# Optimization experiments

Hardware: AMD Instinct MI355X
Metric: run time of the kernel (lower is better)

Reference implementation:

```python
import jax, jax.numpy as jnp
import numpy as np

NUM_HEADS = 32
NUM_KV_HEADS = 8
HEAD_DIM = 128
HIDDEN = 4096
ROPE_THETA = 10000.0
RMS_EPS = 1e-6


def setup_inputs() -> dict:
    key = jax.random.key(0)
    k1, k2, k3 = jax.random.split(key, 3)
    T = 2048
    qkv_out = (NUM_HEADS + 2 * NUM_KV_HEADS) * HEAD_DIM  # 6144
    return {
        "positions": jnp.arange(T, dtype=jnp.int64),
        "hidden_states": jax.random.normal(k1, (T, HIDDEN), dtype=jnp.float32),
        "wqkv": jax.random.normal(k2, (qkv_out, HIDDEN), dtype=jnp.float32) * 0.02,
        "wo": jax.random.normal(k3, (HIDDEN, NUM_HEADS * HEAD_DIM), dtype=jnp.float32) * 0.02,
        "q_norm_w": jnp.ones((HEAD_DIM,), dtype=jnp.float32),
        "k_norm_w": jnp.ones((HEAD_DIM,), dtype=jnp.float32),
    }


def _rms_norm(x, w):
    # per-head RMSNorm over last dim, computed in fp32 (matches Dots1RMSNorm)
    xf = x.astype(jnp.float32)
    var = jnp.mean(xf * xf, axis=-1, keepdims=True)
    return (w * (xf * jax.lax.rsqrt(var + RMS_EPS))).astype(x.dtype)


def _rope(x, positions):
    # NeoX-style rotary: rotate halves. x: [T, H, D]
    half = HEAD_DIM // 2
    inv_freq = 1.0 / (ROPE_THETA ** (jnp.arange(0, half, dtype=jnp.float32) / half))
    ang = positions.astype(jnp.float32)[:, None] * inv_freq  # [T, half]
    cos = jnp.cos(ang)[:, None, :]  # [T,1,half]
    sin = jnp.sin(ang)[:, None, :]
    x1, x2 = x[..., :half], x[..., half:]
    return jnp.concatenate([x1 * cos - x2 * sin, x2 * cos + x1 * sin], axis=-1)


def reference(positions, hidden_states, wqkv, wo, q_norm_w, k_norm_w):
    T = hidden_states.shape[0]
    q_size = NUM_HEADS * HEAD_DIM
    kv_size = NUM_KV_HEADS * HEAD_DIM
    qkv = hidden_states @ wqkv.T  # [T, q_size + 2*kv_size]
    q = qkv[:, :q_size].reshape(T, NUM_HEADS, HEAD_DIM)
    k = qkv[:, q_size:q_size + kv_size].reshape(T, NUM_KV_HEADS, HEAD_DIM)
    v = qkv[:, q_size + kv_size:].reshape(T, NUM_KV_HEADS, HEAD_DIM)

    q = _rms_norm(q, q_norm_w)
    k = _rms_norm(k, k_norm_w)
    q = _rope(q, positions)
    k = _rope(k, positions)

    # GQA: expand kv heads to query heads (group of 4)
    group = NUM_HEADS // NUM_KV_HEADS
    k = jnp.repeat(k, group, axis=1)  # [T, H, D]
    v = jnp.repeat(v, group, axis=1)

    scale = HEAD_DIM ** -0.5
    scores = jnp.einsum('thd,shd->hts', q, k) * scale  # [H, T, T]
    causal = positions[:, None] >= positions[None, :]
    scores = jnp.where(causal[None, :, :], scores, jnp.finfo(scores.dtype).min)
    probs = jax.nn.softmax(scores, axis=-1)
    attn = jnp.einsum('hts,shd->thd', probs, v)  # [T, H, D]
    out = attn.reshape(T, NUM_HEADS * HEAD_DIM) @ wo.T  # [T, HIDDEN]
    return out
```

## Files before the change

kernel.cpp:

```cpp
#include <hip/hip_runtime.h>


#define T_SEQ 2048
#define HID   4096
#define NH    32
#define NKVH  8
#define HD    128
#define QKVN  6144
#define QSZ   4096
#define QKN   5120

typedef unsigned short u16;
typedef __attribute__((ext_vector_type(8))) short short8;
typedef __attribute__((ext_vector_type(4))) float floatx4;

__device__ __forceinline__ float bf2f(u16 u) {
  union { unsigned int i; float f; } c; c.i = ((unsigned int)u) << 16; return c.f;
}
__device__ __forceinline__ u16 f2bf(float f) {
  union { float f; unsigned int i; } c; c.f = f;
  unsigned int u = c.i;
  return (u16)((u + 0x7FFFu + ((u >> 16) & 1u)) >> 16);
}
__device__ __forceinline__ floatx4 mfma16(short8 a, short8 b, floatx4 c) {
  return __builtin_amdgcn_mfma_f32_16x16x32_bf16(a, b, c, 0, 0, 0);
}

#define GLD16(g, l) __builtin_amdgcn_global_load_lds( \
    (__attribute__((address_space(1))) unsigned int*)(g), \
    (__attribute__((address_space(3))) unsigned int*)(l), 16, 0, 0)

__global__ __launch_bounds__(256) void cvt3_kernel(
    const float* __restrict__ s0, const float* __restrict__ s1,
    const float* __restrict__ s2, u16* __restrict__ d0, u16* __restrict__ d1,
    u16* __restrict__ d2, int n0, int n1, int n2) {
  int total = n0 + n1 + n2;
  int stride = gridDim.x * 256;
  for (int i = blockIdx.x * 256 + threadIdx.x; i < total; i += stride) {
    const float* s; u16* d; int j = i;
    if (j < n0)           { s = s0; d = d0; }
    else if (j < n0 + n1) { j -= n0; s = s1; d = d1; }
    else                  { j -= n0 + n1; s = s2; d = d2; }
    float4 v = ((const float4*)s)[j];
    ushort4 o;
    o.x = f2bf(v.x); o.y = f2bf(v.y); o.z = f2bf(v.z); o.w = f2bf(v.w);
    ((ushort4*)d)[j] = o;
  }
}

template <int MODE>
__global__ __launch_bounds__(256, 2) void gemm_bt(const u16* __restrict__ A,
    const u16* __restrict__ B, void* __restrict__ Cv, u16* __restrict__ VT,
    int mtiles, int K, int ldC) {
  __shared__ __attribute__((aligned(16))) u16 As[128 * 64];
  __shared__ __attribute__((aligned(16))) u16 Bs[128 * 64];
  const int tid = threadIdx.x;
  const int wave = tid >> 6, lane = tid & 63;
  const int lq = lane >> 4, lc = lane & 15;
  const int wm = wave >> 1, wn = wave & 1;
  const int by = blockIdx.x % mtiles, bx = blockIdx.x / mtiles;
  const int m0 = by * 128, n0 = bx * 128;

  floatx4 acc[4][4];
#pragma unroll
  for (int i = 0; i < 4; ++i)
#pragma unroll
    for (int j = 0; j < 4; ++j) acc[i][j] = {0.f, 0.f, 0.f, 0.f};

  int arow[4], brow[4];
#pragma unroll
  for (int i = 0; i < 4; ++i) {
    arow[i] = wm * 64 + i * 16 + lc;
    brow[i] = wn * 64 + i * 16 + lc;
  }

  const u16* asrc[4]; const u16* bsrc[4];
#pragma unroll
  for (int r = 0; r < 4; ++r) {
    int L = r * 256 + tid;
    int mm = L >> 3;
    int cc = (L & 7) ^ (mm & 7);
    asrc[r] = A + (size_t)(m0 + mm) * K + cc * 8;
    bsrc[r] = B + (size_t)(n0 + mm) * K + cc * 8;
  }

  for (int k0 = 0; k0 < K; k0 += 64) {
#pragma unroll
    for (int r = 0; r < 4; ++r) {
      GLD16(asrc[r] + k0, As + (r * 256 + wave * 64) * 8);
      GLD16(bsrc[r] + k0, Bs + (r * 256 + wave * 64) * 8);
    }
    __syncthreads();
#pragma unroll
    for (int kb = 0; kb < 2; ++kb) {
      short8 af[4], bfr[4];
#pragma unroll
      for (int mi = 0; mi < 4; ++mi)
        af[mi] = *(const short8*)&As[arow[mi] * 64 + (((kb * 4 + lq) ^ (arow[mi] & 7)) * 8)];
#pragma unroll
      for (int ni = 0; ni < 4; ++ni)
        bfr[ni] = *(const short8*)&Bs[brow[ni] * 64 + (((kb * 4 + lq) ^ (brow[ni] & 7)) * 8)];
#pragma unroll
      for (int mi = 0; mi < 4; ++mi)
#pragma unroll
        for (int ni = 0; ni < 4; ++ni)
          acc[mi][ni] = mfma16(af[mi], bfr[ni], acc[mi][ni]);
    }
    __syncthreads();
  }

  if (MODE == 1 && n0 >= 5120) {
#pragma unroll
    for (int mi = 0; mi < 4; ++mi) {
      int row = m0 + wm * 64 + mi * 16 + lq * 4;
#pragma unroll
      for (int ni = 0; ni < 4; ++ni) {
        int rel = n0 + wn * 64 + ni * 16 + lc - 5120;
        ushort4 u;
        u.x = f2bf(acc[mi][ni][0]); u.y = f2bf(acc[mi][ni][1]);
        u.z = f2bf(acc[mi][ni][2]); u.w = f2bf(acc[mi][ni][3]);
        *(ushort4*)&VT[(size_t)rel * T_SEQ + row] = u;
      }
    }
  } else {
#pragma unroll
    for (int mi = 0; mi < 4; ++mi) {
      int row = m0 + wm * 64 + mi * 16 + lq * 4;
#pragma unroll
      for (int ni = 0; ni < 4; ++ni) {
        int col = n0 + wn * 64 + ni * 16 + lc;
#pragma unroll
        for (int r = 0; r < 4; ++r) {
          if (MODE == 1)
            ((u16*)Cv)[(size_t)(row + r) * ldC + col] = f2bf(acc[mi][ni][r]);
          else
            ((float*)Cv)[(size_t)(row + r) * ldC + col] = acc[mi][ni][r];
        }
      }
    }
  }
}

__global__ __launch_bounds__(256) void norm_rope_kernel(const u16* __restrict__ qk,
    const float* __restrict__ qw, const float* __restrict__ kw,
    u16* __restrict__ Qo, u16* __restrict__ Ko) {
  const int t = blockIdx.x;
  const int hs = blockIdx.y * 4 + (threadIdx.x >> 6);
  const int l = threadIdx.x & 63;
  const bool isq = hs < NH;
  const int col0 = isq ? hs * HD : QSZ + (hs - NH) * HD;
  const u16* src = qk + (size_t)t * QKN + col0;
  float x1 = bf2f(src[l]);
  float x2 = bf2f(src[l + 64]);
  float ss = x1 * x1 + x2 * x2;
#pragma unroll
  for (int m = 1; m < 64; m <<= 1) ss += __shfl_xor(ss, m);
  float rstd = rsqrtf(ss * (1.0f / HD) + 1e-6f);
  const float* w = isq ? qw : kw;
  float n1 = x1 * rstd * w[l];
  float n2 = x2 * rstd * w[l + 64];
  float inv = exp2f((float)l * -0.20762050593045158f);
  float ang = (float)t * inv;
  float s, c;
  __sincosf(ang, &s, &c);
  float o1 = n1 * c - n2 * s;
  float o2 = n2 * c + n1 * s;
  if (isq) {
    o1 *= 0.08838834764831845f; o2 *= 0.08838834764831845f;
    u16* dst = Qo + ((size_t)hs * T_SEQ + t) * HD;
    dst[l] = f2bf(o1); dst[l + 64] = f2bf(o2);
  } else {
    u16* dst = Ko + ((size_t)(hs - NH) * T_SEQ + t) * HD;
    dst[l] = f2bf(o1); dst[l + 64] = f2bf(o2);
  }
}

__global__ __launch_bounds__(256, 2) void attn_kernel(const u16* __restrict__ Qg,
    const u16* __restrict__ Kg, const u16* __restrict__ VTg, u16* __restrict__ Og) {
  __shared__ __attribute__((aligned(16))) u16 Ks[8192];
  __shared__ __attribute__((aligned(16))) u16 Vs[2][8192];
  __shared__ __attribute__((aligned(16))) u16 Ps[8192];

  const int bid = blockIdx.x;
  const int h = bid & 31;
  const int qq = bid >> 5;
  const int qt = (qq < 8) ? (15 - qq) : (qq - 8);
  const int kvh = h >> 2;
  const int tid = threadIdx.x;
  const int wave = tid >> 6, lane = tid & 63;
  const int lq = lane >> 4, lc = lane & 15;

  const u16* kbase[4];
  const u16* vbase[4];
#pragma unroll
  for (int i = 0; i < 4; ++i) {
    int L = i * 256 + tid;
    int s = L >> 4, cp = L & 15;
    kbase[i] = Kg + ((size_t)kvh * T_SEQ + s) * HD + ((cp ^ (s & 15)) * 8);
    int d = L >> 3, cv = L & 7;
    vbase[i] = VTg + ((size_t)kvh * HD + d) * T_SEQ + ((cv ^ (d & 7)) * 8);
  }

  short8 qf[2][4];
#pragma unroll
  for (int mb = 0; mb < 2; ++mb)
#pragma unroll
    for (int ks = 0; ks < 4; ++ks) {
      int t = qt * 128 + wave * 32 + mb * 16 + lc;
      qf[mb][ks] = *(const short8*)&Qg[((size_t)h * T_SEQ + t) * HD + ks * 32 + lq * 8];
    }

  short8 ones;
#pragma unroll
  for (int j = 0; j < 8; ++j) ones[j] = (short)0x3F80;

  floatx4 of[2][8];
  floatx4 lacc[2];
#pragma unroll
  for (int mb = 0; mb < 2; ++mb) {
    lacc[mb] = {0.f, 0.f, 0.f, 0.f};
#pragma unroll
    for (int db = 0; db < 8; ++db) of[mb][db] = {0.f, 0.f, 0.f, 0.f};
  }

  const int ktmax = 2 * qt + 1;
  const int t0g = qt * 128 + wave * 32;
  const int wave_tmax = t0g + 31;

#pragma unroll
  for (int i = 0; i < 4; ++i) {
    GLD16(kbase[i], Ks + (i * 256 + wave * 64) * 8);
    GLD16(vbase[i], Vs[0] + (i * 256 + wave * 64) * 8);
  }

  for (int kt = 0; kt <= ktmax; ++kt) {
    __syncthreads();
    if (kt + 1 <= ktmax) {
      u16* vd = Vs[(kt + 1) & 1] + (size_t)wave * 64 * 8;
#pragma unroll
      for (int i = 0; i < 4; ++i)
        GLD16(vbase[i] + (kt + 1) * 64, vd + i * 256 * 8);
    }
    const bool active = (kt * 64) <= wave_tmax;
    if (active) {
      floatx4 sf[2][4];
#pragma unroll
      for (int mb = 0; mb < 2; ++mb)
#pragma unroll
        for (int nb = 0; nb < 4; ++nb) sf[mb][nb] = {0.f, 0.f, 0.f, 0.f};
#pragma unroll
      for (int ks = 0; ks < 4; ++ks) {
        short8 kf[4];
#pragma unroll
        for (int nb = 0; nb < 4; ++nb)
          kf[nb] = *(const short8*)&Ks[(nb * 16 + lc) * 128 + ((4 * ks + lq) ^ lc) * 8];
#pragma unroll
        for (int mb = 0; mb < 2; ++mb)
#pragma unroll
          for (int nb = 0; nb < 4; ++nb)
            sf[mb][nb] = mfma16(kf[nb], qf[mb][ks], sf[mb][nb]);
      }
      const bool nm = (kt * 64 + 63) > t0g;
#pragma unroll
      for (int mb = 0; mb < 2; ++mb) {
        const int trow = wave * 32 + mb * 16 + lc;
        const int tg = qt * 128 + trow;
#pragma unroll
        for (int nb = 0; nb < 4; ++nb) {
          ushort4 u;
          float p0 = __expf(sf[mb][nb][0]);
          float p1 = __expf(sf[mb][nb][1]);
          float p2 = __expf(sf[mb][nb][2]);
          float p3 = __expf(sf[mb][nb][3]);
          if (nm) {
            int sg = kt * 64 + nb * 16 + lq * 4;
            p0 = (sg + 0 <= tg) ? p0 : 0.f;
            p1 = (sg + 1 <= tg) ? p1 : 0.f;
            p2 = (sg + 2 <= tg) ? p2 : 0.f;
            p3 = (sg + 3 <= tg) ? p3 : 0.f;
          }
          u.x = f2bf(p0); u.y = f2bf(p1); u.z = f2bf(p2); u.w = f2bf(p3);
          int c = 2 * nb + (lq >> 1);
          *(ushort4*)&Ps[trow * 64 + ((c ^ (trow & 7)) * 8) + (lq & 1) * 4] = u;
        }
      }
    }
    __syncthreads();
    if (kt + 1 <= ktmax) {
      u16* kd = Ks + (size_t)wave * 64 * 8;
#pragma unroll
      for (int i = 0; i < 4; ++i)
        GLD16(kbase[i] + (size_t)(kt + 1) * 8192, kd + i * 256 * 8);
    }
    if (active) {
      const u16* vb = Vs[kt & 1];
      short8 pf[2][2];
#pragma unroll
      for (int mb = 0; mb < 2; ++mb)
#pragma unroll
        for (int k2 = 0; k2 < 2; ++k2) {
          int trow = wave * 32 + mb * 16 + lc;
          pf[mb][k2] =
              *(const short8*)&Ps[trow * 64 + (((4 * k2 + lq) ^ (lc & 7)) * 8)];
        }
#pragma unroll
      for (int k2 = 0; k2 < 2; ++k2) {
#pragma unroll
        for (int db = 0; db < 8; ++db) {
          short8 vf =
              *(const short8*)&vb[(db * 16 + lc) * 64 + (((4 * k2 + lq) ^ (lc & 7)) * 8)];
          of[0][db] = mfma16(pf[0][k2], vf, of[0][db]);
          of[1][db] = mfma16(pf[1][k2], vf, of[1][db]);
        }
        lacc[0] = mfma16(pf[0][k2], ones, lacc[0]);
        lacc[1] = mfma16(pf[1][k2], ones, lacc[1]);
      }
    }
  }
#pragma unroll
  for (int mb = 0; mb < 2; ++mb)
#pragma unroll
    for (int r = 0; r < 4; ++r) {
      float inv = 1.f / lacc[mb][r];
      int tg = qt * 128 + wave * 32 + mb * 16 + lq * 4 + r;
#pragma unroll
      for (int db = 0; db < 8; ++db)
        Og[(size_t)tg * QSZ + h * HD + db * 16 + lc] = f2bf(of[mb][db][r] * inv);
    }
}

extern "C" void kernel_launch(void* const* d_in, const int* in_sizes, int n_in,
                              void* d_out, int out_size, void* d_ws, size_t ws_size,
                              hipStream_t stream) {
  (void)in_sizes; (void)n_in; (void)out_size; (void)ws_size;
  const float* hidden = (const float*)d_in[1];
  const float* wqkv   = (const float*)d_in[2];
  const float* wo     = (const float*)d_in[3];
  const float* qw     = (const float*)d_in[4];
  const float* kw     = (const float*)d_in[5];
  float* out = (float*)d_out;
  char* ws = (char*)d_ws;

  u16* h_bf    = (u16*)(ws + 0);
  u16* wq_bf   = (u16*)(ws + 16777216);
  u16* wo_bf   = (u16*)(ws + 67108864);
  u16* vT_bf   = (u16*)(ws + 100663296);
  u16* qk_bf   = (u16*)(ws + 104857600);
  u16* q_bf    = (u16*)(ws + 16777216);
  u16* k_bf    = (u16*)(ws + 33554432);
  u16* attn_bf = (u16*)(ws + 0);

  cvt3_kernel<<<8192, 256, 0, stream>>>(
      hidden, wqkv, wo, h_bf, wq_bf, wo_bf,
      T_SEQ * HID / 4, QKVN * HID / 4, HID * QSZ / 4);

  gemm_bt<1><<<768, 256, 0, stream>>>(h_bf, wq_bf, qk_bf, vT_bf,
                                      T_SEQ / 128, HID, QKN);

  norm_rope_kernel<<<dim3(T_SEQ, 10), 256, 0, stream>>>(
      qk_bf, qw, kw, q_bf, k_bf);

  attn_kernel<<<512, 256, 0, stream>>>(q_bf, k_bf, vT_bf, attn_bf);

  gemm_bt<0><<<512, 256, 0, stream>>>(attn_bf, wo_bf, out, vT_bf,
                                      T_SEQ / 128, HID, QSZ);
}
```

Baseline: 482.8 us.

## Replace QKV GEMM with 256x256 eight-phase pipelined kernel and XCD-aware block remap

Adds a new QKV projection GEMM that uses 256x256 tiles, 512 threads and double-buffered LDS. Each K-step is split into eight phases that interleave global-to-LDS loads with MFMA quadrants, using explicit barriers, waitcnt and setprio to overlap memory with compute. The existing gemm_bt also gets a block-index remap that spreads consecutive tiles across the eight XCDs for better L2 locality, which affects the output projection GEMM. The larger tile reduces global traffic per FLOP but launches only 192 blocks and relies on delicate hand scheduling.

Result: slower. 534.0 us (+10.6%).

```diff
diff --git a/kernel.cpp b/kernel.cpp
--- a/kernel.cpp
+++ b/kernel.cpp
@@ -58,7 +58,8 @@
   const int wave = tid >> 6, lane = tid & 63;
   const int lq = lane >> 4, lc = lane & 15;
   const int wm = wave >> 1, wn = wave & 1;
-  const int by = blockIdx.x % mtiles, bx = blockIdx.x / mtiles;
+  const int id = ((int)blockIdx.x & 7) * ((int)gridDim.x >> 3) + ((int)blockIdx.x >> 3);
+  const int by = id % mtiles, bx = id / mtiles;
   const int m0 = by * 128, n0 = bx * 128;
 
   floatx4 acc[4][4];
@@ -136,6 +137,137 @@
           else
             ((float*)Cv)[(size_t)(row + r) * ldC + col] = acc[mi][ni][r];
         }
+      }
+    }
+  }
+}
+
+#define SGA(BUF, H, S) do { \
+    GLD16(apt[H][0] + (size_t)(S) * 64, As + (BUF) * 16384 + aoff[H][0]); \
+    GLD16(apt[H][1] + (size_t)(S) * 64, As + (BUF) * 16384 + aoff[H][1]); \
+  } while (0)
+#define SGB(BUF, H, S) do { \
+    GLD16(bpt[H][0] + (size_t)(S) * 64, Bs + (BUF) * 16384 + boff[H][0]); \
+    GLD16(bpt[H][1] + (size_t)(S) * 64, Bs + (BUF) * 16384 + boff[H][1]); \
+  } while (0)
+#define VM6 asm volatile("s_waitcnt vmcnt(6)" ::: "memory")
+
+#define PH(BUF, QM, QN, LA, LB, STAGE, VMW) do { \
+    if (LA) { \
+      _Pragma("unroll") for (int mi = 0; mi < 4; ++mi) { \
+        const u16* ap = As + (BUF) * 16384 + abase + ((QM) * 64 + mi * 16) * 64; \
+        af[mi][0] = *(const short8*)(ap + c0); \
+        af[mi][1] = *(const short8*)(ap + c1); \
+      } \
+    } \
+    if (LB) { \
+      _Pragma("unroll") for (int ni = 0; ni < 2; ++ni) { \
+        const u16* bp = Bs + (BUF) * 16384 + bbase + ((QN) * 32 + ni * 16) * 64; \
+        bfr[ni][0] = *(const short8*)(bp + c0); \
+        bfr[ni][1] = *(const short8*)(bp + c1); \
+      } \
+    } \
+    STAGE; \
+    __builtin_amdgcn_s_barrier(); \
+    asm volatile("s_waitcnt lgkmcnt(0)"); \
+    __builtin_amdgcn_s_setprio(1); \
+    _Pragma("unroll") for (int mi = 0; mi < 4; ++mi) \
+      _Pragma("unroll") for (int ni = 0; ni < 2; ++ni) { \
+        acc[(QM) * 4 + mi][(QN) * 2 + ni] = \
+            mfma16(af[mi][0], bfr[ni][0], acc[(QM) * 4 + mi][(QN) * 2 + ni]); \
+        acc[(QM) * 4 + mi][(QN) * 2 + ni] = \
+            mfma16(af[mi][1], bfr[ni][1], acc[(QM) * 4 + mi][(QN) * 2 + ni]); \
+      } \
+    __builtin_amdgcn_s_setprio(0); \
+    VMW; \
+    __builtin_amdgcn_s_barrier(); \
+  } while (0)
+
+__global__ __launch_bounds__(512, 2) void gemm1_8ph(const u16* __restrict__ A,
+    const u16* __restrict__ B, u16* __restrict__ C, u16* __restrict__ VT) {
+  __shared__ __attribute__((aligned(16))) u16 As[2 * 256 * 64];
+  __shared__ __attribute__((aligned(16))) u16 Bs[2 * 256 * 64];
+  const int tid = threadIdx.x;
+  const int wave = tid >> 6, lane = tid & 63;
+  const int lq = lane >> 4, lc = lane & 15;
+  const int wm = wave >> 2, wn = wave & 3;
+  const int id = ((int)blockIdx.x & 7) * 24 + ((int)blockIdx.x >> 3);
+  const int by = id & 7, bx = id >> 3;
+  const int m0 = by * 256, n0 = bx * 256;
+
+  floatx4 acc[8][4];
+#pragma unroll
+  for (int i = 0; i < 8; ++i)
+#pragma unroll
+    for (int j = 0; j < 4; ++j) acc[i][j] = {0.f, 0.f, 0.f, 0.f};
+
+  const int c0 = (lq ^ (lc & 7)) * 8;
+  const int c1 = ((4 + lq) ^ (lc & 7)) * 8;
+  const int abase = (wm * 128 + lc) * 64;
+  const int bbase = (wn * 64 + lc) * 64;
+
+  const int srow = lane >> 3;
+  const int schunk = ((lane & 7) ^ srow) * 8;
+  const u16* apt[2][2]; const u16* bpt[2][2];
+  int aoff[2][2], boff[2][2];
+#pragma unroll
+  for (int h = 0; h < 2; ++h)
+#pragma unroll
+    for (int i = 0; i < 2; ++i) {
+      int idx = wave * 2 + i;
+      int rba = (idx & 7) + (idx >> 3) * 16 + h * 8;
+      int rbb = (idx & 3) + (idx >> 2) * 8 + h * 4;
+      apt[h][i] = A + (size_t)(m0 + rba * 8 + srow) * HID + schunk;
+      bpt[h][i] = B + (size_t)(n0 + rbb * 8 + srow) * HID + schunk;
+      aoff[h][i] = rba * 512;
+      boff[h][i] = rbb * 512;
+    }
+
+  SGA(0, 0, 0); SGB(0, 0, 0); SGB(0, 1, 0); SGA(0, 1, 0);
+  SGA(1, 0, 1); SGB(1, 1, 1); SGA(1, 1, 1);
+  VM6;
+  __builtin_amdgcn_s_barrier();
+
+  short8 af[4][2];
+  short8 bfr[2][2];
+  for (int j = 0; j < 64; j += 2) {
+    const int s2 = (j + 2 < 63) ? j + 2 : 63;
+    const int s3 = (j + 3 < 63) ? j + 3 : 63;
+    PH(0, 0, 0, 1, 1, SGB(1, 0, j + 1), (void)0);
+    PH(0, 0, 1, 0, 1, SGA(0, 0, s2),    (void)0);
+    PH(0, 1, 1, 1, 0, SGB(0, 1, s2),    (void)0);
+    PH(0, 1, 0, 0, 1, SGA(0, 1, s2),    VM6);
+    PH(1, 0, 0, 1, 1, SGB(0, 0, s2),    (void)0);
+    PH(1, 0, 1, 0, 1, SGA(1, 0, s3),    (void)0);
+    PH(1, 1, 1, 1, 0, SGB(1, 1, s3),    (void)0);
+    PH(1, 1, 0, 0, 1, SGA(1, 1, s3),    VM6);
+  }
+
+  asm volatile("s_waitcnt vmcnt(0)" ::: "memory");
+
+  if (n0 >= 5120) {
+#pragma unroll
+    for (int mi = 0; mi < 8; ++mi) {
+      int row = m0 + wm * 128 + mi * 16 + lq * 4;
+#pragma unroll
+      for (int ni = 0; ni < 4; ++ni) {
+        int rel = n0 + wn * 64 + ni * 16 + lc - 5120;
+        ushort4 u;
+        u.x = f2bf(acc[mi][ni][0]); u.y = f2bf(acc[mi][ni][1]);
+        u.z = f2bf(acc[mi][ni][2]); u.w = f2bf(acc[mi][ni][3]);
+        *(ushort4*)&VT[(size_t)rel * T_SEQ + row] = u;
+      }
+    }
+  } else {
+#pragma unroll
+    for (int mi = 0; mi < 8; ++mi) {
+      int row = m0 + wm * 128 + mi * 16 + lq * 4;
+#pragma unroll
+      for (int ni = 0; ni < 4; ++ni) {
+        int col = n0 + wn * 64 + ni * 16 + lc;
+#pragma unroll
+        for (int r = 0; r < 4; ++r)
+          C[(size_t)(row + r) * QKN + col] = f2bf(acc[mi][ni][r]);
       }
     }
   }
@@ -354,8 +486,7 @@
       hidden, wqkv, wo, h_bf, wq_bf, wo_bf,
       T_SEQ * HID / 4, QKVN * HID / 4, HID * QSZ / 4);
 
-  gemm_bt<1><<<768, 256, 0, stream>>>(h_bf, wq_bf, qk_bf, vT_bf,
-                                      T_SEQ / 128, HID, QKN);
+  gemm1_8ph<<<192, 512, 0, stream>>>(h_bf, wq_bf, qk_bf, vT_bf);
 
   norm_rope_kernel<<<dim3(T_SEQ, 10), 256, 0, stream>>>(
       qk_bf, qw, kw, q_bf, k_bf);
```
